# Kernel tuning notes

Measured on AMD Instinct MI355X. Metric: run time of the kernel, lower is better.

## Reference

```python
import jax, jax.numpy as jnp
import numpy as np

N_HEADS, N_KV, HEAD_DIM = 16, 4, 64
DIM = 4096
LATENT = N_HEADS * HEAD_DIM   # 1024
KV_DIM = N_KV * HEAD_DIM      # 256
KSZ = 3


def _causal_conv1d(x, w, b, groups):
    # x: [B,S,C]; w: [Cout, Cin//groups, K]; causal left padding (K-1)
    y = jax.lax.conv_general_dilated(
        x.transpose(0, 2, 1), w, window_strides=(1,),
        padding=[(w.shape[-1] - 1, 0)], feature_group_count=groups,
        dimension_numbers=('NCH', 'OIH', 'NCH'))
    return (y + b[None, :, None]).transpose(0, 2, 1)


def _rope(x, cos, sin):
    # x: [B,H,S,D] interleaved pairs; cos/sin: [1,1,S,D//2]
    x1, x2 = x[..., ::2], x[..., 1::2]
    out = jnp.stack([x1 * cos - x2 * sin, x1 * sin + x2 * cos], axis=-1)
    return out.reshape(x.shape)


def _l2norm(x):
    n = jnp.sqrt(jnp.sum(x * x, axis=-1, keepdims=True))
    return x / jnp.maximum(n, 1e-12)


def setup_inputs() -> dict:
    key = jax.random.key(0)
    ks = jax.random.split(key, 12)
    sc = 0.02
    x = jax.random.normal(ks[0], (2, 2048, DIM), jnp.float32)
    w_qkv = jax.random.normal(ks[1], (LATENT + 2 * KV_DIM, DIM), jnp.float32) * sc
    w_o = jax.random.normal(ks[2], (DIM, LATENT), jnp.float32) * sc
    qc1_w = jax.random.normal(ks[3], (LATENT, LATENT // N_HEADS, KSZ), jnp.float32) * sc
    qc1_b = jnp.zeros((LATENT,), jnp.float32)
    qc2_w = jax.random.normal(ks[4], (LATENT, LATENT, KSZ), jnp.float32) * sc
    qc2_b = jnp.zeros((LATENT,), jnp.float32)
    kc1_w = jax.random.normal(ks[5], (KV_DIM, KV_DIM // N_KV, KSZ), jnp.float32) * sc
    kc1_b = jnp.zeros((KV_DIM,), jnp.float32)
    kc2_w = jax.random.normal(ks[6], (KV_DIM, KV_DIM, KSZ), jnp.float32) * sc
    kc2_b = jnp.zeros((KV_DIM,), jnp.float32)
    key_temp = jnp.full((1,), float(HEAD_DIM) ** 0.5, jnp.float32)
    return dict(x=x, w_qkv=w_qkv, w_o=w_o, qc1_w=qc1_w, qc1_b=qc1_b,
                qc2_w=qc2_w, qc2_b=qc2_b, kc1_w=kc1_w, kc1_b=kc1_b,
                kc2_w=kc2_w, kc2_b=kc2_b, key_temp=key_temp)


def _forward(x, w_qkv, w_o, qc1_w, qc1_b, qc2_w, qc2_b, kc1_w, kc1_b, kc2_w, kc2_b, key_temp):
    B, S, _ = x.shape
    qkv = x @ w_qkv.T  # [B,S,LATENT+2*KV_DIM]
    q = qkv[..., :LATENT]
    k = qkv[..., LATENT:LATENT + KV_DIM]
    # value shift: first half current token, second half previous token (0 at t=0)
    half = KV_DIM // 2
    v_curr = qkv[..., LATENT + KV_DIM:LATENT + KV_DIM + half]
    v_prev = qkv[..., LATENT + KV_DIM + half:]
    v = jnp.concatenate([v_curr, jnp.pad(v_prev[:, :-1, :], ((0, 0), (1, 0), (0, 0)))], axis=-1)
    q_pre, k_pre = q, k
    # grouped causal conv sequences on q and k
    q = _causal_conv1d(_causal_conv1d(q, qc1_w, qc1_b, N_HEADS), qc2_w, qc2_b, 1)
    k = _causal_conv1d(_causal_conv1d(k, kc1_w, kc1_b, N_KV), kc2_w, kc2_b, 1)
    # qk-mean coupling (n_groups = 4 branch)
    q_mean = q_pre.reshape(B, S, N_HEADS, HEAD_DIM).mean(axis=2)  # [B,S,hd]
    k_mean = k_pre.reshape(B, S, N_KV, HEAD_DIM).mean(axis=2)
    q = q.reshape(B, S, N_HEADS, HEAD_DIM) + 0.5 * k_mean[:, :, None, :]
    k = k.reshape(B, S, N_KV, HEAD_DIM) + 0.5 * q_mean[:, :, None, :]
    q = q.transpose(0, 2, 1, 3)                                   # [B,H,S,d]
    k = k.transpose(0, 2, 1, 3)                                   # [B,Hkv,S,d]
    v = v.reshape(B, S, N_KV, HEAD_DIM).transpose(0, 2, 1, 3)
    # qk-norm with learned key temperature
    q = _l2norm(q)
    k = _l2norm(k) * key_temp
    # RoPE (interleaved pairs)
    inv = 1.0 / (10000.0 ** (jnp.arange(0, HEAD_DIM, 2, dtype=jnp.float32) / HEAD_DIM))
    ang = jnp.arange(S, dtype=jnp.float32)[:, None] * inv[None, :]  # [S,d/2]
    cos, sin = jnp.cos(ang)[None, None], jnp.sin(ang)[None, None]
    q = _rope(q, cos, sin)
    k = _rope(k, cos, sin)
    # GQA: each kv head repeated n_groups times contiguously
    kg = jnp.repeat(k, N_HEADS // N_KV, axis=1)
    vg = jnp.repeat(v, N_HEADS // N_KV, axis=1)
    scale = HEAD_DIM ** -0.5
    scores = jnp.einsum('bhqd,bhkd->bhqk', q, kg) * scale
    causal = jnp.tril(jnp.ones((S, S), dtype=bool))
    scores = jnp.where(causal[None, None], scores, jnp.finfo(scores.dtype).min)
    attn = jax.nn.softmax(scores, axis=-1)
    out = jnp.einsum('bhqk,bhkd->bhqd', attn, vg)
    out = out.transpose(0, 2, 1, 3).reshape(B, S, LATENT)
    return out @ w_o.T  # output_scale = 1.0


def reference(x, w_qkv, w_o, qc1_w, qc1_b, qc2_w, qc2_b, kc1_w, kc1_b, kc2_w, kc2_b, key_temp):
    return _forward(x, w_qkv, w_o, qc1_w, qc1_b, qc2_w, qc2_b, kc1_w, kc1_b, kc2_w, kc2_b, key_temp)
```

## Files before the change

kernel.cpp:

```cpp
#include <hip/hip_runtime.h>
#include <hip/hip_bf16.h>
#include <cstddef>

#define NB 2
#define SEQ 2048
#define DIMX 4096
#define NH 16
#define NKV 4
#define HD 64
#define LATENT 1024
#define KVD 256
#define QKVN 1536
#define BS (NB*SEQ)
#define SP (SEQ+2)

typedef __attribute__((ext_vector_type(8))) short short8v;
typedef __attribute__((ext_vector_type(4))) float f32x4;
typedef __attribute__((ext_vector_type(4))) unsigned short ushort4v;
typedef __attribute__((ext_vector_type(4))) unsigned int uint4v;

static __device__ __forceinline__ unsigned short f2bf(float f) {
    union { float f; unsigned u; } v; v.f = f;
    unsigned r = v.u + 0x7fffu + ((v.u >> 16) & 1u);
    return (unsigned short)(r >> 16);
}

static __device__ __forceinline__ unsigned cvt_pk_bf16(float lo, float hi) {
    unsigned r;
    asm("v_cvt_pk_bf16_f32 %0, %1, %2" : "=v"(r) : "v"(lo), "v"(hi));
    return r;
}

static __device__ __forceinline__ void gload_lds16(const unsigned short* g, unsigned short* l) {
    __builtin_amdgcn_global_load_lds((const __attribute__((address_space(1))) void*)g,
                                     (__attribute__((address_space(3))) void*)l, 16, 0, 0);
}

__global__ __launch_bounds__(256)
void cast_f2b(const float* __restrict__ in, unsigned short* __restrict__ out, int n4)
{
    const int i = blockIdx.x * 256 + threadIdx.x;
    if (i < n4) {
        const float4 v = *reinterpret_cast<const float4*>(in + (size_t)i * 4);
        ushort4v o = {f2bf(v.x), f2bf(v.y), f2bf(v.z), f2bf(v.w)};
        *reinterpret_cast<ushort4v*>(out + (size_t)i * 4) = o;
    }
}

__global__ __launch_bounds__(256)
void w3reorder(const float* __restrict__ w, unsigned short* __restrict__ wr, int O, int I)
{
    const int idx = blockIdx.x * 256 + threadIdx.x;
    if (idx < O * I * 3) {
        const int o = idx / (I * 3), rem = idx % (I * 3);
        const int j = rem / I, c = rem % I;
        wr[idx] = f2bf(w[(size_t)o * I * 3 + c * 3 + j]);
    }
}

__global__ __launch_bounds__(256)
void zero_pad(unsigned short* __restrict__ pq, unsigned short* __restrict__ pk)
{
    const int t = blockIdx.x * 256 + threadIdx.x;
    if (t < 2 * 2 * LATENT) {
        const int b = t / (2 * LATENT), r = (t % (2 * LATENT)) / LATENT, c = t % LATENT;
        pq[((size_t)b * SP + r) * LATENT + c] = 0;
    }
    if (t < 2 * 2 * KVD) {
        const int b = t / (2 * KVD), r = (t % (2 * KVD)) / KVD, c = t % KVD;
        pk[((size_t)b * SP + r) * KVD + c] = 0;
    }
}

__global__ __launch_bounds__(256)
void add2(const float* __restrict__ p0, const float* __restrict__ p1,
          const float* __restrict__ bias, float* __restrict__ out, int n4, int ncols)
{
    const int i = blockIdx.x * 256 + threadIdx.x;
    if (i < n4) {
        const float4 a = *reinterpret_cast<const float4*>(p0 + (size_t)i * 4);
        const float4 b = *reinterpret_cast<const float4*>(p1 + (size_t)i * 4);
        float4 o = make_float4(a.x + b.x, a.y + b.y, a.z + b.z, a.w + b.w);
        if (bias != nullptr) {
            const int col = (i * 4) % ncols;
            o.x += bias[col]; o.y += bias[col + 1]; o.z += bias[col + 2]; o.w += bias[col + 3];
        }
        *reinterpret_cast<float4*>(out + (size_t)i * 4) = o;
    }
}

__global__ __launch_bounds__(256)
void rope_tab(float2* __restrict__ tab)
{
    const int idx = blockIdx.x * 256 + threadIdx.x;
    const int s = idx >> 5, i = idx & 31;
    const float inv = powf(10000.f, -(float)(2 * i) * (1.f / HD));
    const float ang = (float)s * inv;
    tab[idx] = make_float2(cosf(ang), sinf(ang));
}

template<int CONV>
__global__ __launch_bounds__(256)
void gemm_bf16(const unsigned short* __restrict__ A, const unsigned short* __restrict__ W,
               const float* __restrict__ bias, float* __restrict__ C,
               int M, int N, int K, int Cch, int klen, size_t pstride)
{
    __shared__ unsigned short Abuf[2][128 * 32];
    __shared__ unsigned short Bbuf[2][128 * 32];
    const int gx = gridDim.x;
    const int nwg = gx * gridDim.y;
    const int lin = blockIdx.y * gx + blockIdx.x;
    const int swz = (lin & 7) * (nwg >> 3) + (lin >> 3);
    const int n0 = (swz % gx) * 128, m0 = (swz / gx) * 128;
    const int koff = blockIdx.z * klen;
    C += (size_t)blockIdx.z * pstride;
    const int tid = threadIdx.x;
    const int wave = tid >> 6, lane = tid & 63;
    const int lg = lane >> 4, lr = lane & 15;
    const int wm = (wave & 1) * 64, wn = (wave >> 1) * 64;
    const int sr = wave * 32 + (lane >> 2);
    const int sc = (lane & 3) * 8;
    const int bb = m0 / SEQ, s0 = m0 % SEQ;

    const int NT = klen / 32;
    f32x4 acc[4][4];
    #pragma unroll
    for (int i = 0; i < 4; i++)
        #pragma unroll
        for (int j = 0; j < 4; j++) acc[i][j] = (f32x4){0.f, 0.f, 0.f, 0.f};

    auto stage = [&](int buf, int kt) {
        const int k0 = koff + kt * 32;
        const unsigned short* ga0;
        if (!CONV) {
            ga0 = A + (size_t)(m0 + sr) * K + k0 + sc;
        } else {
            const int j = k0 / Cch, c0 = k0 - j * Cch;
            ga0 = A + (size_t)(bb * SP + s0 + j + sr) * Cch + c0 + sc;
        }
        const unsigned short* gb0 = W + (size_t)(n0 + sr) * K + k0 + sc;
        const size_t astep = (size_t)16 * (CONV ? Cch : K);
        #pragma unroll
        for (int i = 0; i < 2; i++) {
            gload_lds16(ga0 + i * astep, &Abuf[buf][(wave * 2 + i) * 512]);
            gload_lds16(gb0 + (size_t)i * 16 * K, &Bbuf[buf][(wave * 2 + i) * 512]);
        }
    };

    stage(0, 0);
    __syncthreads();
    int cur = 0;
    for (int kt = 0; kt < NT; ++kt) {
        if (kt + 1 < NT) stage(cur ^ 1, kt + 1);
        short8v af[4], bf[4];
        #pragma unroll
        for (int mi = 0; mi < 4; mi++)
            af[mi] = *reinterpret_cast<const short8v*>(&Abuf[cur][(wm + mi * 16 + lr) * 32 + lg * 8]);
        #pragma unroll
        for (int ni = 0; ni < 4; ni++)
            bf[ni] = *reinterpret_cast<const short8v*>(&Bbuf[cur][(wn + ni * 16 + lr) * 32 + lg * 8]);
        #pragma unroll
        for (int mi = 0; mi < 4; mi++)
            #pragma unroll
            for (int ni = 0; ni < 4; ni++)
                acc[mi][ni] = __builtin_amdgcn_mfma_f32_16x16x32_bf16(af[mi], bf[ni], acc[mi][ni], 0, 0, 0);
        __syncthreads();
        cur ^= 1;
    }

    #pragma unroll
    for (int ni = 0; ni < 4; ni++) {
        const int col = n0 + wn + ni * 16 + lr;
        const float bv = bias ? bias[col] : 0.f;
        #pragma unroll
        for (int mi = 0; mi < 4; mi++)
            #pragma unroll
            for (int r = 0; r < 4; r++)
                C[(size_t)(m0 + wm + mi * 16 + lg * 4 + r) * N + col] = acc[mi][ni][r] + bv;
    }
}

__global__ __launch_bounds__(256)
void conv1_grouped(const float* __restrict__ qkv, int coloff,
                   const float* __restrict__ w, const float* __restrict__ bias,
                   unsigned short* __restrict__ out, int CH)
{
    const int t0 = blockIdx.x * 64;
    const int b  = blockIdx.y;
    const int g  = blockIdx.z;
    __shared__ float xs[66][64];
    for (int idx = threadIdx.x; idx < 66 * 64; idx += 256) {
        const int i = idx >> 6, ic = idx & 63;
        const int tt = t0 + i - 2;
        xs[i][ic] = (tt >= 0) ? qkv[(size_t)(b * SEQ + tt) * QKVN + coloff + g * 64 + ic] : 0.f;
    }
    __syncthreads();
    const int oc = threadIdx.x & 63;
    const int ibase = (threadIdx.x >> 6) * 16;
    float acc[16];
    const float bv = bias[g * 64 + oc];
    #pragma unroll
    for (int i = 0; i < 16; i++) acc[i] = bv;
    const float* wp = w + (size_t)(g * 64 + oc) * 192;
    for (int ic = 0; ic < 64; ic++) {
        const float w0 = wp[ic * 3 + 0], w1 = wp[ic * 3 + 1], w2 = wp[ic * 3 + 2];
        float xv[18];
        #pragma unroll
        for (int r = 0; r < 18; r++) xv[r] = xs[ibase + r][ic];
        #pragma unroll
        for (int i = 0; i < 16; i++) acc[i] += w0 * xv[i] + w1 * xv[i + 1] + w2 * xv[i + 2];
    }
    #pragma unroll
    for (int i = 0; i < 16; i++)
        out[((size_t)b * SP + 2 + t0 + ibase + i) * CH + g * 64 + oc] = f2bf(acc[i]);
}

__global__ __launch_bounds__(64)
void meanv_kernel(const float* __restrict__ qkv, float* __restrict__ qmean,
                  float* __restrict__ kmean, unsigned short* __restrict__ vRow)
{
    const int t = blockIdx.x, d = threadIdx.x;
    const int b = t >> 11, s = t & (SEQ - 1);
    const float* row = qkv + (size_t)t * QKVN;
    float qs = 0.f;
    #pragma unroll
    for (int h = 0; h < NH; h++) qs += row[h * 64 + d];
    qmean[t * 64 + d] = qs * (1.f / NH);
    float ks = 0.f;
    #pragma unroll
    for (int h = 0; h < NKV; h++) ks += row[LATENT + h * 64 + d];
    kmean[t * 64 + d] = ks * (1.f / NKV);
    #pragma unroll
    for (int g = 0; g < NKV; g++) {
        const int c = g * 64 + d;
        float v;
        if (c < 128) v = row[LATENT + KVD + c];
        else         v = (s > 0) ? qkv[(size_t)(t - 1) * QKVN + LATENT + KVD + 128 + (c - 128)] : 0.f;
        vRow[((size_t)(b * NKV + g) * SEQ + s) * 64 + d] = f2bf(v);
    }
}

__global__ __launch_bounds__(256)
void vtrans(const unsigned short* __restrict__ vRow, unsigned short* __restrict__ vTb)
{
    const int s0 = blockIdx.x * 64;
    const int bg = blockIdx.y;
    __shared__ unsigned short t[64][72];
    const int tid = threadIdx.x;
    {
        const int r = tid >> 2, c0 = (tid & 3) * 16;
        const unsigned short* p = vRow + ((size_t)bg * SEQ + s0 + r) * 64 + c0;
        const short8v a = *reinterpret_cast<const short8v*>(p);
        const short8v bv = *reinterpret_cast<const short8v*>(p + 8);
        #pragma unroll
        for (int j = 0; j < 8; j++) { t[r][c0 + j] = (unsigned short)a[j]; t[r][c0 + 8 + j] = (unsigned short)bv[j]; }
    }
    __syncthreads();
    {
        const int d = tid >> 2, ss = (tid & 3) * 16;
        short8v o0, o1;
        #pragma unroll
        for (int j = 0; j < 8; j++) { o0[j] = (short)t[ss + j][d]; o1[j] = (short)t[ss + 8 + j][d]; }
        unsigned short* op = vTb + ((size_t)bg * 64 + d) * SEQ + s0 + ss;
        *reinterpret_cast<short8v*>(op) = o0;
        *reinterpret_cast<short8v*>(op + 8) = o1;
    }
}

__global__ __launch_bounds__(64)
void qk_final(const float* __restrict__ qc2a, const float* __restrict__ qc2b,
              const float* __restrict__ kc2a, const float* __restrict__ kc2b,
              const float* __restrict__ qbias, const float* __restrict__ kbias,
              const float* __restrict__ qmean, const float* __restrict__ kmean,
              const float* __restrict__ key_temp, const float2* __restrict__ rtab,
              unsigned short* __restrict__ qTb, unsigned short* __restrict__ kTb)
{
    const int t = blockIdx.x, hh = blockIdx.y, d = threadIdx.x;
    const int b = t >> 11, s = t & (SEQ - 1);
    float val;
    if (hh < NH) {
        const size_t off = (size_t)t * LATENT + hh * 64 + d;
        val = qc2a[off] + qc2b[off] + qbias[hh * 64 + d] + 0.5f * kmean[t * 64 + d];
    } else {
        const size_t off = (size_t)t * KVD + (hh - NH) * 64 + d;
        val = kc2a[off] + kc2b[off] + kbias[(hh - NH) * 64 + d] + 0.5f * qmean[t * 64 + d];
    }
    float ss = val * val;
    #pragma unroll
    for (int off = 32; off >= 1; off >>= 1) ss += __shfl_xor(ss, off);
    const float n = sqrtf(ss);
    val = val / fmaxf(n, 1e-12f);
    if (hh >= NH) val *= key_temp[0];
    const float2 cs = rtab[s * 32 + (d >> 1)];
    const float cv = cs.x, sv = cs.y;
    const float partner = __shfl_xor(val, 1);
    const float x1 = (d & 1) ? partner : val;
    const float x2 = (d & 1) ? val : partner;
    const float o = (d & 1) ? (x1 * sv + x2 * cv) : (x1 * cv - x2 * sv);
    if (hh < NH) qTb[((size_t)(b * NH + hh) * SEQ + s) * 64 + d] = f2bf(o);
    else         kTb[((size_t)(b * NKV + (hh - NH)) * SEQ + s) * 64 + d] = f2bf(o);
}

__global__ __launch_bounds__(256)
void attn_mfma(const unsigned short* __restrict__ qTb, const unsigned short* __restrict__ kTb,
               const unsigned short* __restrict__ vTb, unsigned short* __restrict__ attn_out)
{
    const int wg = blockIdx.x;
    int bh, blk;
    if (wg < 256) {
        const int xcd = wg & 7, i = wg >> 3;
        bh = (xcd << 2) | (i >> 3);
        blk = 15 - (i & 7);
    } else {
        const int u = wg - 256;
        const int xcd = u & 7, i = u >> 3;
        bh = (xcd << 2) | (i >> 3);
        blk = i & 7;
    }
    const int b = bh >> 4, h = bh & 15, g = h >> 2;
    const int tid = threadIdx.x;
    const int wave = tid >> 6, lane = tid & 63;
    const int lg = lane >> 4, lr = lane & 15;
    const int qt = blk * 4 + wave;
    const int q0 = qt * 32;
    const int ctot2 = (blk + 1) * 2;

    __shared__ __align__(16) unsigned short SB[2][16][512];

    short8v qf[2][2];
    const unsigned short* qbase = qTb + ((size_t)(b * NH + h) * SEQ + q0) * 64;
    #pragma unroll
    for (int mf = 0; mf < 2; mf++)
        #pragma unroll
        for (int dc = 0; dc < 2; dc++)
            qf[mf][dc] = *reinterpret_cast<const short8v*>(qbase + (size_t)(mf * 16 + lr) * 64 + dc * 32 + lg * 8);

    f32x4 acc[2][4];
    float lsum[2] = {0.f, 0.f};
    #pragma unroll
    for (int mf = 0; mf < 2; mf++)
        #pragma unroll
        for (int dt = 0; dt < 4; dt++) acc[mf][dt] = (f32x4){0.f, 0.f, 0.f, 0.f};

    const unsigned short* kbase = kTb + (size_t)(b * NKV + g) * SEQ * 64;
    const unsigned short* vbase = vTb + (size_t)(b * NKV + g) * 64 * SEQ;
    const float EC = 0.125f * 1.44269504f;
    const int src01 = ((lg & 1) << 5) + lr;
    const int src23 = src01 + 16;
    const bool hi = (lg >= 2);

    auto stage64 = [&](int buf, int cc) {
        const int kb = cc * 64;
        #pragma unroll
        for (int i = 0; i < 4; i++) {
            const int ch = wave * 4 + i;
            const int st = ch >> 3, chl = ch & 7;
            const int k0 = kb + st * 32;
            const unsigned short* src;
            if (chl < 4) src = kbase + (size_t)(k0 + (chl >> 1) * 16 + lr) * 64 + (chl & 1) * 32 + lg * 8;
            else         src = vbase + (size_t)((chl - 4) * 16 + lr) * SEQ + k0 + lg * 8;
            gload_lds16(src, &SB[buf][ch][lane * 8]);
        }
    };

    stage64(0, 0);
    __syncthreads();
    int cur = 0;
    for (int cc = 0; cc < ctot2; ++cc) {
        if (cc + 1 < ctot2) stage64(cur ^ 1, cc + 1);
        #pragma unroll
        for (int st = 0; st < 2; ++st) {
            const int c = cc * 2 + st;
            if (c > qt) continue;
            const int k0 = c * 32;
            short8v kf[2][2], vf[4];
            #pragma unroll
            for (int kt = 0; kt < 2; kt++)
                #pragma unroll
                for (int dc = 0; dc < 2; dc++)
                    kf[kt][dc] = *reinterpret_cast<const short8v*>(&SB[cur][st * 8 + kt * 2 + dc][lane * 8]);
            #pragma unroll
            for (int dt = 0; dt < 4; dt++)
                vf[dt] = *reinterpret_cast<const short8v*>(&SB[cur][st * 8 + 4 + dt][lane * 8]);

            const bool diag = (c == qt);
            #pragma unroll
            for (int mf = 0; mf < 2; mf++) {
                f32x4 z0 = (f32x4){0.f, 0.f, 0.f, 0.f}, z1 = (f32x4){0.f, 0.f, 0.f, 0.f};
                __builtin_amdgcn_s_setprio(1);
                z0 = __builtin_amdgcn_mfma_f32_16x16x32_bf16(kf[0][0], qf[mf][0], z0, 0, 0, 0);
                z0 = __builtin_amdgcn_mfma_f32_16x16x32_bf16(kf[0][1], qf[mf][1], z0, 0, 0, 0);
                z1 = __builtin_amdgcn_mfma_f32_16x16x32_bf16(kf[1][0], qf[mf][0], z1, 0, 0, 0);
                z1 = __builtin_amdgcn_mfma_f32_16x16x32_bf16(kf[1][1], qf[mf][1], z1, 0, 0, 0);
                __builtin_amdgcn_s_setprio(0);
                float p0[4], p1[4];
                #pragma unroll
                for (int r = 0; r < 4; r++) {
                    p0[r] = exp2f(z0[r] * EC);
                    p1[r] = exp2f(z1[r] * EC);
                }
                if (diag) {
                    const int q = q0 + mf * 16 + lr;
                    #pragma unroll
                    for (int r = 0; r < 4; r++) {
                        if (k0 + 4 * lg + r > q)      p0[r] = 0.f;
                        if (k0 + 16 + 4 * lg + r > q) p1[r] = 0.f;
                    }
                }
                lsum[mf] += (p0[0] + p0[1]) + (p0[2] + p0[3]) + (p1[0] + p1[1]) + (p1[2] + p1[3]);
                const unsigned W00 = cvt_pk_bf16(p0[0], p0[1]);
                const unsigned W01 = cvt_pk_bf16(p0[2], p0[3]);
                const unsigned W10 = cvt_pk_bf16(p1[0], p1[1]);
                const unsigned W11 = cvt_pk_bf16(p1[2], p1[3]);
                const unsigned a0 = __shfl(W00, src01), b0 = __shfl(W10, src01);
                const unsigned a1 = __shfl(W01, src01), b1 = __shfl(W11, src01);
                const unsigned a2 = __shfl(W00, src23), b2 = __shfl(W10, src23);
                const unsigned a3 = __shfl(W01, src23), b3 = __shfl(W11, src23);
                uint4v pw;
                pw.x = hi ? b0 : a0;
                pw.y = hi ? b1 : a1;
                pw.z = hi ? b2 : a2;
                pw.w = hi ? b3 : a3;
                const short8v pa = __builtin_bit_cast(short8v, pw);
                __builtin_amdgcn_s_setprio(1);
                #pragma unroll
                for (int dt = 0; dt < 4; dt++)
                    acc[mf][dt] = __builtin_amdgcn_mfma_f32_16x16x32_bf16(pa, vf[dt], acc[mf][dt], 0, 0, 0);
                __builtin_amdgcn_s_setprio(0);
            }
        }
        __syncthreads();
        cur ^= 1;
    }

    float den[2];
    #pragma unroll
    for (int mf = 0; mf < 2; mf++) {
        float s = lsum[mf];
        s += __shfl_xor(s, 16); s += __shfl_xor(s, 32);
        den[mf] = s;
    }

    #pragma unroll
    for (int mf = 0; mf < 2; mf++) {
        float dinv[4];
        #pragma unroll
        for (int r = 0; r < 4; r++) dinv[r] = 1.f / __shfl(den[mf], 4 * lg + r);
        #pragma unroll
        for (int dt = 0; dt < 4; dt++)
            #pragma unroll
            for (int r = 0; r < 4; r++) {
                const int q = q0 + mf * 16 + 4 * lg + r;
                attn_out[(size_t)(b * SEQ + q) * LATENT + h * 64 + dt * 16 + lr] = f2bf(acc[mf][dt][r] * dinv[r]);
            }
    }
}

extern "C" void kernel_launch(void* const* d_in, const int* in_sizes, int n_in,
                              void* d_out, int out_size, void* d_ws, size_t ws_size,
                              hipStream_t stream)
{
    const float* x       = (const float*)d_in[0];
    const float* w_qkv   = (const float*)d_in[1];
    const float* w_o     = (const float*)d_in[2];
    const float* qc1_w   = (const float*)d_in[3];
    const float* qc1_b   = (const float*)d_in[4];
    const float* qc2_w   = (const float*)d_in[5];
    const float* qc2_b   = (const float*)d_in[6];
    const float* kc1_w   = (const float*)d_in[7];
    const float* kc1_b   = (const float*)d_in[8];
    const float* kc2_w   = (const float*)d_in[9];
    const float* kc2_b   = (const float*)d_in[10];
    const float* key_temp = (const float*)d_in[11];

    char* wsb = (char*)d_ws;
    float* qkv = (float*)wsb;                 wsb += (size_t)BS * QKVN * 4;
    float* qc2 = qkv;
    float* kc2 = (float*)((char*)qkv + (size_t)BS * LATENT * 4);
    unsigned short* pq  = (unsigned short*)wsb;  wsb += (size_t)NB * SP * LATENT * 2;
    unsigned short* pk  = (unsigned short*)wsb;  wsb += (size_t)NB * SP * KVD * 2;
    float* qmean = (float*)wsb;  wsb += (size_t)BS * HD * 4;
    float* kmean = (float*)wsb;  wsb += (size_t)BS * HD * 4;
    unsigned short* qTb  = (unsigned short*)wsb;  wsb += (size_t)BS * LATENT * 2;
    unsigned short* kTb  = (unsigned short*)wsb;  wsb += (size_t)BS * KVD * 2;
    unsigned short* vRow = (unsigned short*)wsb;  wsb += (size_t)BS * KVD * 2;
    unsigned short* vTb  = (unsigned short*)wsb;  wsb += (size_t)BS * KVD * 2;
    unsigned short* xb   = (unsigned short*)wsb;  wsb += (size_t)BS * DIMX * 2;
    unsigned short* attnb  = xb;
    unsigned short* qc2wr  = (unsigned short*)((char*)xb + (size_t)BS * LATENT * 2);
    unsigned short* kc2wr  = (unsigned short*)((char*)qc2wr + (size_t)LATENT * LATENT * 3 * 2);
    unsigned short* wqkvb = (unsigned short*)wsb;  wsb += (size_t)QKVN * DIMX * 2;
    unsigned short* wob   = wqkvb;

    const size_t QKV_PS = (size_t)BS * QKVN;
    float* qc2p1 = (float*)((char*)d_ws + 67512320);
    float* kc2p1 = (float*)((char*)d_ws + (size_t)BS * QKVN * 4);
    const size_t QC2_PS = (size_t)(qc2p1 - qc2);
    const size_t KC2_PS = (size_t)(kc2p1 - kc2);
    float2* rtab = (float2*)vRow;

    float* outp = (float*)d_out;

    cast_f2b<<<dim3(BS * DIMX / 4 / 256), 256, 0, stream>>>(x, xb, BS * DIMX / 4);
    cast_f2b<<<dim3(QKVN * DIMX / 4 / 256), 256, 0, stream>>>(w_qkv, wqkvb, QKVN * DIMX / 4);
    gemm_bf16<0><<<dim3(QKVN / 128, BS / 128, 2), 256, 0, stream>>>(xb, wqkvb, nullptr, qkv, BS, QKVN, DIMX, 0, DIMX / 2, QKV_PS);
    add2<<<dim3(BS * QKVN / 4 / 256), 256, 0, stream>>>(qkv, qkv + QKV_PS, nullptr, qkv, BS * QKVN / 4, 4);
    cast_f2b<<<dim3(DIMX * LATENT / 4 / 256), 256, 0, stream>>>(w_o, wob, DIMX * LATENT / 4);
    w3reorder<<<dim3((LATENT * LATENT * 3 + 255) / 256), 256, 0, stream>>>(qc2_w, qc2wr, LATENT, LATENT);
    w3reorder<<<dim3((KVD * KVD * 3 + 255) / 256), 256, 0, stream>>>(kc2_w, kc2wr, KVD, KVD);
    meanv_kernel<<<dim3(BS), 64, 0, stream>>>(qkv, qmean, kmean, vRow);
    vtrans<<<dim3(SEQ / 64, NB * NKV), 256, 0, stream>>>(vRow, vTb);
    rope_tab<<<dim3(SEQ * 32 / 256), 256, 0, stream>>>(rtab);
    zero_pad<<<dim3(16), 256, 0, stream>>>(pq, pk);
    conv1_grouped<<<dim3(SEQ / 64, NB, NH),  256, 0, stream>>>(qkv, 0,      qc1_w, qc1_b, pq, LATENT);
    conv1_grouped<<<dim3(SEQ / 64, NB, NKV), 256, 0, stream>>>(qkv, LATENT, kc1_w, kc1_b, pk, KVD);
    gemm_bf16<1><<<dim3(LATENT / 128, BS / 128, 2), 256, 0, stream>>>(pq, qc2wr, nullptr, qc2, BS, LATENT, LATENT * 3, LATENT, LATENT * 3 / 2, QC2_PS);
    gemm_bf16<1><<<dim3(KVD / 128, BS / 128, 2), 256, 0, stream>>>(pk, kc2wr, nullptr, kc2, BS, KVD, KVD * 3, KVD, KVD * 3 / 2, KC2_PS);
    qk_final<<<dim3(BS, NH + NKV), 64, 0, stream>>>(qc2, qc2p1, kc2, kc2p1, qc2_b, kc2_b,
                                                    qmean, kmean, key_temp, rtab, qTb, kTb);
    attn_mfma<<<dim3(512), 256, 0, stream>>>(qTb, kTb, vTb, attnb);
    gemm_bf16<0><<<dim3(DIMX / 128, BS / 128, 1), 256, 0, stream>>>(attnb, wob, nullptr, outp, BS, DIMX, LATENT, 0, LATENT, 0);
}
```

Baseline: 382.3 us.

## Add 256x256-tile triple-buffered bf16 GEMM for QKV and output projections

Adds a new GEMM kernel with 256x256 output tiles, 512 threads, a three-stage LDS buffer of async global-to-LDS loads, and prefetch interleaved with MFMA issue under raised wave priority. The QKV projection and the output projection now use it instead of the 128x128 double-buffered kernel. Larger tiles raise arithmetic intensity and cut global traffic, and the deeper pipeline hides more load latency. In exchange the grids get smaller (QKV: 6x16x2=192 blocks, out: 16x16=256), which may underfill the CUs, and register and LDS use per block rise (96KB LDS, 128 accumulators per thread).

```diff
diff --git a/kernel.cpp b/kernel.cpp
--- a/kernel.cpp
+++ b/kernel.cpp
@@ -97,6 +97,89 @@
     const float inv = powf(10000.f, -(float)(2 * i) * (1.f / HD));
     const float ang = (float)s * inv;
     tab[idx] = make_float2(cosf(ang), sinf(ang));
+}
+
+__global__ __launch_bounds__(512)
+void gemm256(const unsigned short* __restrict__ A, const unsigned short* __restrict__ W,
+             float* __restrict__ C, int M, int N, int K, int klen, size_t pstride)
+{
+    __shared__ unsigned short SA[3][256 * 32];
+    __shared__ unsigned short SBm[3][256 * 32];
+    const int gx = gridDim.x;
+    const int nwg = gx * gridDim.y;
+    const int lin = blockIdx.y * gx + blockIdx.x;
+    const int swz = (lin & 7) * (nwg >> 3) + (lin >> 3);
+    const int n0 = (swz % gx) * 256, m0 = (swz / gx) * 256;
+    const int koff = blockIdx.z * klen;
+    C += (size_t)blockIdx.z * pstride;
+    const int tid = threadIdx.x;
+    const int wid = tid >> 6, lane = tid & 63;
+    const int lg = lane >> 4, lr = lane & 15;
+    const int wm = wid >> 2, wn = wid & 3;
+    const int NT = klen / 32;
+
+    f32x4 acc[8][4];
+    #pragma unroll
+    for (int i = 0; i < 8; i++)
+        #pragma unroll
+        for (int j = 0; j < 4; j++) acc[i][j] = (f32x4){0.f, 0.f, 0.f, 0.f};
+
+    auto stage1 = [&](int buf, int kt, int i) {
+        const int c = i * 512 + tid;
+        const int row = c >> 2, slot = c & 3;
+        const int scol = (slot ^ ((row >> 1) & 3)) << 3;
+        gload_lds16(A + (size_t)(m0 + row) * K + koff + kt * 32 + scol, &SA[buf][c * 8]);
+        gload_lds16(W + (size_t)(n0 + row) * K + koff + kt * 32 + scol, &SBm[buf][c * 8]);
+    };
+
+    stage1(0, 0, 0); stage1(0, 0, 1);
+    stage1(1, 1, 0); stage1(1, 1, 1);
+
+    for (int kt = 0; kt < NT; ++kt) {
+        const int cur = kt % 3;
+        const int nb = (kt + 2) % 3;
+        const bool pre = (kt + 2) < NT;
+        if (kt + 1 < NT) asm volatile("s_waitcnt vmcnt(4)" ::: "memory");
+        else             asm volatile("s_waitcnt vmcnt(0)" ::: "memory");
+        __builtin_amdgcn_sched_barrier(0);
+        __builtin_amdgcn_s_barrier();
+        asm volatile("" ::: "memory");
+
+        short8v bfr[4];
+        #pragma unroll
+        for (int ni = 0; ni < 4; ni++) {
+            const int br = wn * 64 + ni * 16 + lr;
+            bfr[ni] = *reinterpret_cast<const short8v*>(&SBm[cur][br * 32 + ((lg ^ ((br >> 1) & 3)) << 3)]);
+        }
+        #pragma unroll
+        for (int q = 0; q < 4; q++) {
+            if (q == 0 && pre) stage1(nb, kt + 2, 0);
+            if (q == 2 && pre) stage1(nb, kt + 2, 1);
+            const int ar0 = wm * 128 + (2 * q) * 16 + lr;
+            const int ar1 = ar0 + 16;
+            const short8v a0 = *reinterpret_cast<const short8v*>(&SA[cur][ar0 * 32 + ((lg ^ ((ar0 >> 1) & 3)) << 3)]);
+            const short8v a1 = *reinterpret_cast<const short8v*>(&SA[cur][ar1 * 32 + ((lg ^ ((ar1 >> 1) & 3)) << 3)]);
+            __builtin_amdgcn_s_setprio(1);
+            #pragma unroll
+            for (int ni = 0; ni < 4; ni++) {
+                acc[2 * q][ni]     = __builtin_amdgcn_mfma_f32_16x16x32_bf16(a0, bfr[ni], acc[2 * q][ni], 0, 0, 0);
+                acc[2 * q + 1][ni] = __builtin_amdgcn_mfma_f32_16x16x32_bf16(a1, bfr[ni], acc[2 * q + 1][ni], 0, 0, 0);
+            }
+            __builtin_amdgcn_s_setprio(0);
+        }
+        asm volatile("" ::: "memory");
+        __builtin_amdgcn_s_barrier();
+    }
+
+    #pragma unroll
+    for (int ni = 0; ni < 4; ni++) {
+        const int col = n0 + wn * 64 + ni * 16 + lr;
+        #pragma unroll
+        for (int mi = 0; mi < 8; mi++)
+            #pragma unroll
+            for (int r = 0; r < 4; r++)
+                C[(size_t)(m0 + wm * 128 + mi * 16 + lg * 4 + r) * N + col] = acc[mi][ni][r];
+    }
 }
 
 template<int CONV>
@@ -503,7 +586,7 @@
 
     cast_f2b<<<dim3(BS * DIMX / 4 / 256), 256, 0, stream>>>(x, xb, BS * DIMX / 4);
     cast_f2b<<<dim3(QKVN * DIMX / 4 / 256), 256, 0, stream>>>(w_qkv, wqkvb, QKVN * DIMX / 4);
-    gemm_bf16<0><<<dim3(QKVN / 128, BS / 128, 2), 256, 0, stream>>>(xb, wqkvb, nullptr, qkv, BS, QKVN, DIMX, 0, DIMX / 2, QKV_PS);
+    gemm256<<<dim3(QKVN / 256, BS / 256, 2), 512, 0, stream>>>(xb, wqkvb, qkv, BS, QKVN, DIMX, DIMX / 2, QKV_PS);
     add2<<<dim3(BS * QKVN / 4 / 256), 256, 0, stream>>>(qkv, qkv + QKV_PS, nullptr, qkv, BS * QKVN / 4, 4);
     cast_f2b<<<dim3(DIMX * LATENT / 4 / 256), 256, 0, stream>>>(w_o, wob, DIMX * LATENT / 4);
     w3reorder<<<dim3((LATENT * LATENT * 3 + 255) / 256), 256, 0, stream>>>(qc2_w, qc2wr, LATENT, LATENT);
@@ -519,5 +602,5 @@
     qk_final<<<dim3(BS, NH + NKV), 64, 0, stream>>>(qc2, qc2p1, kc2, kc2p1, qc2_b, kc2_b,
                                                     qmean, kmean, key_temp, rtab, qTb, kTb);
     attn_mfma<<<dim3(512), 256, 0, stream>>>(qTb, kTb, vTb, attnb);
-    gemm_bf16<0><<<dim3(DIMX / 128, BS / 128, 1), 256, 0, stream>>>(attnb, wob, nullptr, outp, BS, DIMX, LATENT, 0, LATENT, 0);
-}
+    gemm256<<<dim3(DIMX / 256, BS / 256, 1), 512, 0, stream>>>(attnb, wob, outp, BS, DIMX, LATENT, LATENT, 0);
+}
```

After: 396.9 us. 1.04x slower.
